# Performance work log

Hardware: AMD Instinct MI355X
Metric: run time of the kernel (lower is better)

## Reference

```python
import jax, jax.numpy as jnp
import numpy as np

NUM_EMBEDDINGS = 1024
EMBEDDING_DIM = 64
COMMITMENT_COST = 0.25


def setup_inputs() -> dict:
    key = jax.random.key(0)
    k1, k2 = jax.random.split(key)
    latents = jax.random.normal(k1, (64, EMBEDDING_DIM, 32, 32), dtype=jnp.float32)
    # torch init: uniform_(-1/num_embeddings, 1/num_embeddings)
    codebook = jax.random.uniform(
        k2, (NUM_EMBEDDINGS, EMBEDDING_DIM), dtype=jnp.float32,
        minval=-1.0 / NUM_EMBEDDINGS, maxval=1.0 / NUM_EMBEDDINGS)
    return {"latents": latents, "codebook": codebook}


def reference(latents, codebook):
    B, C, H, W = latents.shape
    K = codebook.shape[0]
    x = jnp.transpose(latents, (0, 2, 3, 1))            # [B,H,W,C]
    x_flat = x.reshape(-1, C)                            # [N,C]
    # squared euclidean distances [N,K]
    dist = (jnp.sum(x_flat ** 2, axis=1, keepdims=True)
            + jnp.sum(codebook ** 2, axis=1)
            - 2.0 * x_flat @ codebook.T)
    idx = jnp.argmin(dist, axis=1)                       # [N] int
    q_flat = codebook[idx]                               # [N,C]
    q = q_flat.reshape(x.shape)                          # [B,H,W,C]
    e_loss = jnp.mean((jax.lax.stop_gradient(q) - x) ** 2)
    q_loss = jnp.mean((q - jax.lax.stop_gradient(x)) ** 2)
    vq_loss = q_loss + COMMITMENT_COST * e_loss
    # straight-through estimator
    q_st = x + jax.lax.stop_gradient(q - x)
    quantized = jnp.transpose(q_st, (0, 3, 1, 2))        # [B,C,H,W]
    # perplexity from code usage histogram
    N = x_flat.shape[0]
    avg_probs = jnp.zeros((K,), dtype=jnp.float32).at[idx].add(1.0) / N
    perplexity = jnp.exp(-jnp.sum(avg_probs * jnp.log(avg_probs + 1e-10)))
    encoding_indices = idx.reshape(B, H, W)
    return (vq_loss, quantized, perplexity, encoding_indices)
```

## Files before the change

kernel.cpp:

```cpp
#include <hip/hip_runtime.h>

#define N_PTS   65536
#define K_CODES 1024
#define C_DIM   64
#define HW      1024
#define Q_ELEMS 4194304
#define NBLOCKS 1024

#define OUT_Q_OFF 1
#define OUT_P_OFF 4194305
#define OUT_I_OFF 4194306

#define WS_HIST 0
#define WS_CNT  4096
#define WS_SSE  4104
#define WS_CSUM 4112
#define WS_CBP  8208

#define EPS_A_W 7.5e-5f
#define EPS_T_W 2.0e-4f

typedef float f32x16 __attribute__((ext_vector_type(16)));
typedef short bf16x8 __attribute__((ext_vector_type(8)));

__device__ __forceinline__ unsigned short bf16rn(float f) {
    unsigned int u = __float_as_uint(f);
    return (unsigned short)((u + 0x7FFFu + ((u >> 16) & 1u)) >> 16);
}
__device__ __forceinline__ float bf16tof(unsigned short h) {
    return __uint_as_float(((unsigned int)h) << 16);
}

__device__ __forceinline__ float np_pairwise_sumsq64(const float* a) {
    float r[8];
    #pragma unroll
    for (int j = 0; j < 8; ++j) r[j] = __fmul_rn(a[j], a[j]);
    #pragma unroll
    for (int i = 8; i < 64; i += 8) {
        #pragma unroll
        for (int j = 0; j < 8; ++j)
            r[j] = __fadd_rn(r[j], __fmul_rn(a[i + j], a[i + j]));
    }
    return __fadd_rn(__fadd_rn(__fadd_rn(r[0], r[1]), __fadd_rn(r[2], r[3])),
                     __fadd_rn(__fadd_rn(r[4], r[5]), __fadd_rn(r[6], r[7])));
}

__global__ void vq_prep(const float* __restrict__ cb, float* __restrict__ csum,
                        unsigned short* __restrict__ cbp) {
    __shared__ float rs[32 * 65];
    __shared__ float csl[32];
    const int t = blockIdx.x, tid = threadIdx.x;
    const float* src = cb + (size_t)t * 2048;
    for (int i = tid; i < 2048; i += 256) {
        int row = i >> 6, d = i & 63;
        rs[row * 65 + d] = src[i];
    }
    __syncthreads();
    if (tid < 32) {
        float cs = np_pairwise_sumsq64(&rs[tid * 65]);
        csum[t * 32 + tid] = cs;
        csl[tid] = cs;
    }
    __syncthreads();
    if (tid < 64) {
        int l31 = tid & 31, half = tid >> 5;
        const float* r = &rs[l31 * 65];
        unsigned short* dst = cbp + (size_t)t * 9 * 512;
        #pragma unroll
        for (int c = 0; c < 4; ++c) {
            bf16x8 h8, l8;
            #pragma unroll
            for (int j = 0; j < 8; ++j) {
                float f = r[c * 16 + half * 8 + j];
                unsigned short h = bf16rn(f);
                h8[j] = (short)h;
                l8[j] = (short)bf16rn(f - bf16tof(h));
            }
            *(bf16x8*)(dst + (size_t)(c * 2 + 0) * 512 + tid * 8) = h8;
            *(bf16x8*)(dst + (size_t)(c * 2 + 1) * 512 + tid * 8) = l8;
        }
        bf16x8 c8;
        #pragma unroll
        for (int j = 0; j < 8; ++j) c8[j] = 0;
        if (half == 0) c8[0] = (short)bf16rn(-0.5f * csl[l31]);
        *(bf16x8*)(dst + (size_t)8 * 512 + tid * 8) = c8;
    }
}

__global__ __launch_bounds__(256, 3) void vq_main(
        const float* __restrict__ latents,
        const float* __restrict__ cb,
        const float* __restrict__ csum,
        const unsigned short* __restrict__ cbp,
        unsigned int* __restrict__ hist,
        double* __restrict__ sse,
        unsigned int* __restrict__ counter,
        float* __restrict__ out) {
    __shared__ float xs[64 * 65];
    __shared__ float tmax[32 * 64];
    __shared__ float sm1[2][64], sm2[2][64];
    __shared__ int   si1[2][64];
    __shared__ float m1f[64];
    __shared__ int   fk[64], ambig[64];
    __shared__ int   acount, lastflag;
    __shared__ double red[256];

    const int tid  = threadIdx.x;
    const int lane = tid & 63, wave = tid >> 6;
    const int chh = wave & 1, pg = wave >> 1;
    const int n0 = blockIdx.x * 64;
    const int b = n0 >> 10, hw0 = n0 & 1023;
    const float* xg = latents + (size_t)b * C_DIM * HW + hw0;

    for (int i = tid; i < 64 * 64; i += 256) {
        int p = i & 63, d = i >> 6;
        xs[p * 65 + d] = xg[(size_t)d * HW + p];
    }
    if (tid == 0) acount = 0;
    __syncthreads();

    const int l31 = lane & 31, half = lane >> 5;
    const int pb = (pg << 5) + l31;
    bf16x8 xh[4], xl[4], x4;
    #pragma unroll
    for (int c = 0; c < 4; ++c)
        #pragma unroll
        for (int j = 0; j < 8; ++j) {
            float f = xs[pb * 65 + c * 16 + half * 8 + j];
            unsigned short h = bf16rn(f);
            xh[c][j] = (short)h;
            xl[c][j] = (short)bf16rn(f - bf16tof(h));
        }
    #pragma unroll
    for (int j = 0; j < 8; ++j) x4[j] = 0;
    if (half == 0) x4[0] = (short)0x3F80;

    float m1 = -3e38f, m2 = -3e38f;
    int i1 = 0;
    const int RC[16] = {0,1,2,3,8,9,10,11,16,17,18,19,24,25,26,27};
    const int rh4 = half * 4;

    for (int t = 0; t < 16; ++t) {
        const int tg = (chh << 4) + t;
        const bf16x8* bp = (const bf16x8*)cbp + (size_t)tg * 576 + lane;
        bf16x8 ch[4], cl[4], ca;
        #pragma unroll
        for (int c = 0; c < 4; ++c) {
            ch[c] = bp[c * 128];
            cl[c] = bp[c * 128 + 64];
        }
        ca = bp[512];
        f32x16 accA, accB1, accB2;
        #pragma unroll
        for (int r = 0; r < 16; ++r) { accA[r] = 0.0f; accB1[r] = 0.0f; accB2[r] = 0.0f; }
        #pragma unroll
        for (int c = 0; c < 4; ++c)
            accA = __builtin_amdgcn_mfma_f32_32x32x16_bf16(ch[c], xh[c], accA, 0, 0, 0);
        accA = __builtin_amdgcn_mfma_f32_32x32x16_bf16(ca, x4, accA, 0, 0, 0);
        #pragma unroll
        for (int c = 0; c < 4; ++c)
            accB1 = __builtin_amdgcn_mfma_f32_32x32x16_bf16(ch[c], xl[c], accB1, 0, 0, 0);
        #pragma unroll
        for (int c = 0; c < 4; ++c)
            accB2 = __builtin_amdgcn_mfma_f32_32x32x16_bf16(cl[c], xh[c], accB2, 0, 0, 0);
        float tl = -3e38f;
        const int tb2 = tg << 5;
        #pragma unroll
        for (int r = 0; r < 16; ++r) {
            float v = __fadd_rn(__fadd_rn(accA[r], accB1[r]), accB2[r]);
            int k = tb2 + RC[r] + rh4;
            m2 = fmaxf(m2, fminf(m1, v));
            i1 = (v > m1) ? k : i1;
            m1 = fmaxf(m1, v);
            tl = fmaxf(tl, v);
        }
        tl = fmaxf(tl, __shfl_xor(tl, 32, 64));
        if (half == 0) tmax[tg * 64 + pb] = tl;
    }
    {
        float m1o = __shfl_xor(m1, 32, 64);
        float m2o = __shfl_xor(m2, 32, 64);
        int   i1o = __shfl_xor(i1, 32, 64);
        m2 = fmaxf(fmaxf(m2, m2o), fminf(m1, m1o));
        i1 = (m1o > m1) ? i1o : i1;
        m1 = fmaxf(m1, m1o);
        if (half == 0) { sm1[chh][pb] = m1; sm2[chh][pb] = m2; si1[chh][pb] = i1; }
    }
    __syncthreads();

    if (tid < 64) {
        float a1 = sm1[0][tid], a2 = sm2[0][tid];
        float b1 = sm1[1][tid], b2 = sm2[1][tid];
        float mm1 = fmaxf(a1, b1);
        float mm2 = fmaxf(fminf(a1, b1), fmaxf(a2, b2));
        m1f[tid] = mm1;
        fk[tid] = (b1 > a1) ? si1[1][tid] : si1[0][tid];
        if (mm2 >= mm1 - EPS_A_W) {
            int a = atomicAdd(&acount, 1);
            ambig[a] = tid;
        }
    }
    __syncthreads();

    for (int a = wave; a < acount; a += 4) {
        int p = ambig[a];
        const float* xrow = &xs[p * 65];
        float Aq = np_pairwise_sumsq64(xrow);
        float thr = m1f[p] - EPS_T_W;
        unsigned long long best = ~0ULL;
        for (int t = 0; t < 32; ++t) {
            if (tmax[t * 64 + p] < thr) continue;
            if (lane < 32) {
                int k = (t << 5) + lane;
                const float* crow = cb + (size_t)k * 64;
                float m = 0.0f;
                #pragma unroll
                for (int d = 0; d < 64; ++d) m = __fmaf_rn(xrow[d], crow[d], m);
                float D = __fsub_rn(__fadd_rn(Aq, csum[k]), __fmul_rn(2.0f, m));
                unsigned long long key =
                    ((unsigned long long)__float_as_uint(D) << 10) | (unsigned)k;
                best = (key < best) ? key : best;
            }
        }
        #pragma unroll
        for (int off = 32; off > 0; off >>= 1) {
            unsigned long long o = __shfl_xor(best, off, 64);
            best = (o < best) ? o : best;
        }
        if (lane == 0) fk[p] = (int)(best & 1023ULL);
    }
    __syncthreads();

    if (tid < 64) {
        int myk = fk[tid];
        out[OUT_I_OFF + n0 + tid] = (float)myk;
        atomicAdd(&hist[myk], 1u);
        const float* crow = cb + (size_t)myk * 64;
        const float* xrow = &xs[tid * 65];
        double e = 0.0;
        #pragma unroll
        for (int d = 0; d < 64; ++d) {
            double df = (double)xrow[d] - (double)crow[d];
            e = fma(df, df, e);
        }
        #pragma unroll
        for (int off = 32; off > 0; off >>= 1) e += __shfl_down(e, off, 64);
        if (tid == 0) atomicAdd(sse, e);
    }
    for (int i = tid; i < 64 * 64; i += 256) {
        int p = i & 63, c = i >> 6;
        out[OUT_Q_OFF + (size_t)b * 65536 + (size_t)c * HW + hw0 + p] =
            cb[(size_t)fk[p] * 64 + c];
    }

    __syncthreads();
    if (tid == 0) lastflag = (atomicAdd(counter, 1u) == NBLOCKS - 1) ? 1 : 0;
    __syncthreads();
    if (lastflag) {
        double s = 0.0;
        for (int i = tid; i < K_CODES; i += 256) {
            double p = (double)atomicAdd(&hist[i], 0u) / (double)N_PTS;
            s += p * log(p + 1e-10);
        }
        red[tid] = s;
        __syncthreads();
        for (int w = 128; w > 0; w >>= 1) {
            if (tid < w) red[tid] += red[tid + w];
            __syncthreads();
        }
        if (tid == 0) {
            out[OUT_P_OFF] = (float)exp(-red[0]);
            double sv = atomicAdd(sse, 0.0);
            out[0] = (float)(1.25 * sv / (double)Q_ELEMS);
        }
    }
}

extern "C" void kernel_launch(void* const* d_in, const int* in_sizes, int n_in,
                              void* d_out, int out_size, void* d_ws, size_t ws_size,
                              hipStream_t stream) {
    const float* latents = (const float*)d_in[0];
    const float* cb      = (const float*)d_in[1];
    float* out = (float*)d_out;
    char* ws = (char*)d_ws;

    unsigned int*   hist    = (unsigned int*)(ws + WS_HIST);
    unsigned int*   counter = (unsigned int*)(ws + WS_CNT);
    double*         sse     = (double*)(ws + WS_SSE);
    float*          csum    = (float*)(ws + WS_CSUM);
    unsigned short* cbp     = (unsigned short*)(ws + WS_CBP);

    hipMemsetAsync(ws, 0, 4112, stream);

    vq_prep <<<32, 256, 0, stream>>>(cb, csum, cbp);
    vq_main <<<NBLOCKS, 256, 0, stream>>>(latents, cb, csum, cbp, hist, sse, counter, out);
}
```

Baseline: 157.3 us.

## Fold workspace zeroing into prep kernel and parallelize SSE/quantized epilogue

Removes the separate hipMemsetAsync by having vq_prep zero the histogram, counter and SSE accumulator. The epilogue now spreads the squared-error computation across all 256 threads, gathering codebook rows coalesced and staging the quantized values in shared memory before the transposed write. The SSE is reduced through shared memory instead of only 64 threads doing 64-element loops. Launch bounds drop from 3 to 2 blocks per SM, giving the compiler more registers at the cost of occupancy.

```diff
diff --git a/kernel.cpp b/kernel.cpp
--- a/kernel.cpp
+++ b/kernel.cpp
@@ -46,10 +46,15 @@
 }
 
 __global__ void vq_prep(const float* __restrict__ cb, float* __restrict__ csum,
-                        unsigned short* __restrict__ cbp) {
+                        unsigned short* __restrict__ cbp,
+                        unsigned int* __restrict__ hist,
+                        unsigned int* __restrict__ counter,
+                        double* __restrict__ sse) {
     __shared__ float rs[32 * 65];
     __shared__ float csl[32];
     const int t = blockIdx.x, tid = threadIdx.x;
+    if (tid < 32) hist[t * 32 + tid] = 0u;
+    if (t == 0 && tid == 0) { *counter = 0u; *sse = 0.0; }
     const float* src = cb + (size_t)t * 2048;
     for (int i = tid; i < 2048; i += 256) {
         int row = i >> 6, d = i & 63;
@@ -87,7 +92,7 @@
     }
 }
 
-__global__ __launch_bounds__(256, 3) void vq_main(
+__global__ __launch_bounds__(256, 2) void vq_main(
         const float* __restrict__ latents,
         const float* __restrict__ cb,
         const float* __restrict__ csum,
@@ -232,25 +237,38 @@
     __syncthreads();
 
     if (tid < 64) {
-        int myk = fk[tid];
-        out[OUT_I_OFF + n0 + tid] = (float)myk;
-        atomicAdd(&hist[myk], 1u);
-        const float* crow = cb + (size_t)myk * 64;
-        const float* xrow = &xs[tid * 65];
+        out[OUT_I_OFF + n0 + tid] = (float)fk[tid];
+        atomicAdd(&hist[fk[tid]], 1u);
+    }
+
+    {
         double e = 0.0;
         #pragma unroll
-        for (int d = 0; d < 64; ++d) {
-            double df = (double)xrow[d] - (double)crow[d];
+        for (int it = 0; it < 16; ++it) {
+            int i = tid + it * 256;
+            int p = i >> 6, c = i & 63;
+            float q = cb[(size_t)fk[p] * 64 + c];
+            float xv = xs[p * 65 + c];
+            double df = (double)xv - (double)q;
             e = fma(df, df, e);
-        }
-        #pragma unroll
-        for (int off = 32; off > 0; off >>= 1) e += __shfl_down(e, off, 64);
-        if (tid == 0) atomicAdd(sse, e);
-    }
-    for (int i = tid; i < 64 * 64; i += 256) {
+            xs[p * 65 + c] = q;
+        }
+        red[tid] = e;
+    }
+    __syncthreads();
+    if (tid < 128) red[tid] += red[tid + 128];
+    __syncthreads();
+    if (tid < 64) {
+        double v = red[tid] + red[tid + 64];
+        #pragma unroll
+        for (int off = 32; off > 0; off >>= 1) v += __shfl_down(v, off, 64);
+        if (tid == 0) atomicAdd(sse, v);
+    }
+    #pragma unroll
+    for (int it = 0; it < 16; ++it) {
+        int i = tid + it * 256;
         int p = i & 63, c = i >> 6;
-        out[OUT_Q_OFF + (size_t)b * 65536 + (size_t)c * HW + hw0 + p] =
-            cb[(size_t)fk[p] * 64 + c];
+        out[OUT_Q_OFF + (size_t)b * 65536 + (size_t)c * HW + hw0 + p] = xs[p * 65 + c];
     }
 
     __syncthreads();
@@ -290,8 +308,6 @@
     float*          csum    = (float*)(ws + WS_CSUM);
     unsigned short* cbp     = (unsigned short*)(ws + WS_CBP);
 
-    hipMemsetAsync(ws, 0, 4112, stream);
-
-    vq_prep <<<32, 256, 0, stream>>>(cb, csum, cbp);
+    vq_prep <<<32, 256, 0, stream>>>(cb, csum, cbp, hist, counter, sse);
     vq_main <<<NBLOCKS, 256, 0, stream>>>(latents, cb, csum, cbp, hist, sse, counter, out);
 }
```

Measured after the change: 152.4 us. -3.1%, faster.
